# Optimization experiments

Hardware: AMD Instinct MI355X
Metric: run time of the kernel (lower is better)

The kernel has to match this reference:

```python
import jax, jax.numpy as jnp
import numpy as np

B, D, K, E = 4096, 2048, 512, 8  # tokens, model dim, kept SVD rank, experts


def setup_inputs() -> dict:
    key = jax.random.key(0)
    ks = jax.random.split(key, 7)
    x = jax.random.normal(ks[0], (B, D), dtype=jnp.float32)
    # frozen base weight (stands in for pretrained_weight)
    W = jax.random.normal(ks[1], (D, D), dtype=jnp.float32) / np.sqrt(D)
    # frozen truncated SVD factors: U_k (D,K) left vecs, V_k (K,D) as sliced in the torch code
    U_k = jnp.linalg.qr(jax.random.normal(ks[2], (D, K), dtype=jnp.float32))[0]
    V_k = jnp.linalg.qr(jax.random.normal(ks[3], (D, K), dtype=jnp.float32))[0].T
    lambda_k = jax.random.normal(ks[4], (E, K), dtype=jnp.float32) * 0.02
    v = jnp.zeros((D,), dtype=jnp.float32)
    router_W1 = jax.random.normal(ks[5], (K, 1), dtype=jnp.float32)
    router_W2 = jax.random.normal(ks[6], (1, E), dtype=jnp.float32)
    return {"x": x, "W": W, "U_k": U_k, "V_k": V_k, "lambda_k": lambda_k,
            "v": v, "router_W1": router_W1, "router_W2": router_W2}


def reference(x, W, U_k, V_k, lambda_k, v, router_W1, router_W2):
    # routing: x @ U_k -> rank-1 router -> softmax over experts
    routing = x @ U_k                                   # (B,K)
    g = jax.nn.softmax((routing @ router_W1) @ router_W2, axis=-1)  # (B,E)
    # per-expert low-rank delta weight, materialized as in the original
    delta_W = jnp.einsum('dk,ek,kn->edn', U_k, lambda_k, V_k)       # (E,D,D)
    W_tot = W[None] + delta_W                           # (E,D,D)
    # F.linear semantics: out = x @ W_tot^T per expert
    expert_out = jnp.einsum('bd,end->ben', x, W_tot)    # (B,E,D)
    out = jnp.einsum('ben,be->bn', expert_out, g)       # gated combine
    return out * (1.0 + v)
```

## Files before the change

### kernel.cpp

```cpp
#include <hip/hip_runtime.h>
#include <hip/hip_bf16.h>
#include <cstdint>

#define B_TOK 4096
#define DDIM  2048
#define KR    512
#define NE    8

using f32x4  = __attribute__((ext_vector_type(4))) float;
using short8 = __attribute__((ext_vector_type(8))) short;
using u16 = unsigned short;

__device__ inline u16 f2bf(float f) {
    union { float f; uint32_t u; } x; x.f = f;
    uint32_t u = x.u;
    return (u16)((u + 0x7fffu + ((u >> 16) & 1u)) >> 16);
}

__device__ inline void gload_lds16(const u16* g, u16* l) {
    __builtin_amdgcn_global_load_lds(
        (const __attribute__((address_space(1))) void*)g,
        (__attribute__((address_space(3))) void*)l, 16, 0, 0);
}

__global__ void cvt_copy2d(const float* __restrict__ src, u16* __restrict__ dst,
                           int rows, int cols4, int src_ld, int dst_ld) {
    int total = rows * cols4;
    for (int i = blockIdx.x * blockDim.x + threadIdx.x; i < total;
         i += gridDim.x * blockDim.x) {
        int r = i / cols4, c = i - r * cols4;
        float4 val = *((const float4*)(src + (size_t)r * src_ld) + c);
        ushort4 o;
        o.x = f2bf(val.x); o.y = f2bf(val.y); o.z = f2bf(val.z); o.w = f2bf(val.w);
        *((ushort4*)(dst + (size_t)r * dst_ld) + c) = o;
    }
}

__global__ void transpose_cvt(const float* __restrict__ src, u16* __restrict__ dst,
                              int src_cols , int dst_ld ) {
    __shared__ float tile[32][33];
    int c0 = blockIdx.x * 32;
    int r0 = blockIdx.y * 32;
    int tx = threadIdx.x, ty = threadIdx.y;
    #pragma unroll
    for (int j = 0; j < 32; j += 8)
        tile[ty + j][tx] = src[(size_t)(r0 + ty + j) * src_cols + c0 + tx];
    __syncthreads();
    #pragma unroll
    for (int j = 0; j < 32; j += 8)
        dst[(size_t)(c0 + ty + j) * dst_ld + r0 + tx] = f2bf(tile[tx][ty + j]);
}

__global__ __launch_bounds__(256)
void router_kernel(const float* __restrict__ rt, const float* __restrict__ W1,
                   const float* __restrict__ W2, const float* __restrict__ lam,
                   u16* __restrict__ Aaug) {
    int b = blockIdx.x;
    int tid = threadIdx.x;
    const float* r = rt + (size_t)b * 1024;

    float p = r[tid] * W1[tid] + r[tid + 256] * W1[tid + 256];
    #pragma unroll
    for (int o = 32; o > 0; o >>= 1) p += __shfl_down(p, o);
    __shared__ float sp[4];
    __shared__ float sbc;
    if ((tid & 63) == 0) sp[tid >> 6] = p;
    __syncthreads();
    if (tid == 0) sbc = sp[0] + sp[1] + sp[2] + sp[3];
    __syncthreads();
    float s = sbc;

    float g[NE]; float mx = -1e30f;
    #pragma unroll
    for (int e = 0; e < NE; e++) { g[e] = s * W2[e]; mx = fmaxf(mx, g[e]); }
    float den = 0.f;
    #pragma unroll
    for (int e = 0; e < NE; e++) { g[e] = expf(g[e] - mx); den += g[e]; }
    float inv = 1.0f / den;

    for (int kk = tid; kk < KR; kk += 256) {
        float mu = 0.f;
        #pragma unroll
        for (int e = 0; e < NE; e++) mu += g[e] * lam[e * KR + kk];
        float m = mu * inv * r[512 + kk];
        Aaug[(size_t)b * 2560 + 2048 + kk] = f2bf(m);
    }
}

template<int BM, int BN, int WGM, int WGN, bool HAS_V>
__global__ __launch_bounds__(256, 2)
void gemm_db(const u16* __restrict__ A, const u16* __restrict__ Bm,
             float* __restrict__ C, const float* __restrict__ v,
             int N, int Kc, int lda, int ldb, int nbx) {
    constexpr int MF = BM / (WGM * 16);
    constexpr int NF = BN / (WGN * 16);
    constexpr int ISSA = BM / 32;
    constexpr int ISSB = BN / 32;
    __shared__ u16 sA[2 * BM * 64];
    __shared__ u16 sB[2 * BN * 64];

    const int tid = threadIdx.x;
    const int wid = tid >> 6, lane = tid & 63;
    const int l15 = lane & 15, l4 = lane >> 4;
    const int wm = wid / WGN, wn = wid % WGN;

    const int nwg = gridDim.x;
    const int id = (blockIdx.x & 7) * (nwg >> 3) + (blockIdx.x >> 3);
    const int row0 = (id / nbx) * BM;
    const int col0 = (id % nbx) * BN;

    const int srow = tid >> 3;
    const int scol = ((tid & 7) ^ (srow & 7)) << 3;
    const u16* gA = A + (size_t)(row0 + srow) * lda + scol;
    const u16* gB = Bm + (size_t)(col0 + srow) * ldb + scol;

    f32x4 acc[MF][NF] = {};
    const int nt = Kc >> 6;

    #pragma unroll
    for (int i = 0; i < ISSA; i++)
        gload_lds16(gA + (size_t)i * 32 * lda, sA + i * 2048 + wid * 512);
    #pragma unroll
    for (int i = 0; i < ISSB; i++)
        gload_lds16(gB + (size_t)i * 32 * ldb, sB + i * 2048 + wid * 512);
    __syncthreads();

    for (int t = 0; t < nt; ++t) {
        const int cur = t & 1;
        if (t + 1 < nt) {
            const int nxt = cur ^ 1;
            const u16* gAk = gA + (size_t)(t + 1) * 64;
            const u16* gBk = gB + (size_t)(t + 1) * 64;
            #pragma unroll
            for (int i = 0; i < ISSA; i++)
                gload_lds16(gAk + (size_t)i * 32 * lda,
                            sA + nxt * BM * 64 + i * 2048 + wid * 512);
            #pragma unroll
            for (int i = 0; i < ISSB; i++)
                gload_lds16(gBk + (size_t)i * 32 * ldb,
                            sB + nxt * BN * 64 + i * 2048 + wid * 512);
        }
        const u16* a0 = sA + cur * BM * 64;
        const u16* b0 = sB + cur * BN * 64;
        #pragma unroll
        for (int kc = 0; kc < 8; kc += 4) {
            short8 af[MF], bv[NF];
            #pragma unroll
            for (int mf = 0; mf < MF; mf++) {
                int row = wm * MF * 16 + mf * 16 + l15;
                int ch = (kc + l4) ^ (row & 7);
                af[mf] = *(const short8*)(a0 + row * 64 + ch * 8);
            }
            #pragma unroll
            for (int nf = 0; nf < NF; nf++) {
                int row = wn * NF * 16 + nf * 16 + l15;
                int ch = (kc + l4) ^ (row & 7);
                bv[nf] = *(const short8*)(b0 + row * 64 + ch * 8);
            }
            #pragma unroll
            for (int mf = 0; mf < MF; mf++)
                #pragma unroll
                for (int nf = 0; nf < NF; nf++)
                    acc[mf][nf] = __builtin_amdgcn_mfma_f32_16x16x32_bf16(
                        af[mf], bv[nf], acc[mf][nf], 0, 0, 0);
        }
        __syncthreads();
    }

    #pragma unroll
    for (int nf = 0; nf < NF; nf++) {
        int col = col0 + wn * NF * 16 + nf * 16 + l15;
        float sc = HAS_V ? (1.0f + v[col]) : 1.0f;
        #pragma unroll
        for (int mf = 0; mf < MF; mf++) {
            int row = row0 + wm * MF * 16 + mf * 16 + l4 * 4;
            #pragma unroll
            for (int r2 = 0; r2 < 4; r2++)
                C[(size_t)(row + r2) * N + col] = acc[mf][nf][r2] * sc;
        }
    }
}

extern "C" void kernel_launch(void* const* d_in, const int* in_sizes, int n_in,
                              void* d_out, int out_size, void* d_ws, size_t ws_size,
                              hipStream_t stream) {
    const float* x   = (const float*)d_in[0];
    const float* W   = (const float*)d_in[1];
    const float* U   = (const float*)d_in[2];
    const float* V   = (const float*)d_in[3];
    const float* lam = (const float*)d_in[4];
    const float* v   = (const float*)d_in[5];
    const float* W1  = (const float*)d_in[6];
    const float* W2  = (const float*)d_in[7];
    float* out = (float*)d_out;

    char* ws = (char*)d_ws;
    u16*   Aaug = (u16*)ws;
    u16*   BigB = (u16*)(ws + 20971520);
    u16*   UVT  = (u16*)(ws + 31457280);
    float* rt   = (float*)(ws + 35651584);

    cvt_copy2d<<<2048, 256, 0, stream>>>(x, Aaug, 4096, 512, 2048, 2560);
    cvt_copy2d<<<2048, 256, 0, stream>>>(W, BigB, 2048, 512, 2048, 2560);
    cvt_copy2d<<<1024, 256, 0, stream>>>(U, BigB + 2048, 2048, 128, 512, 2560);
    cvt_copy2d<<<2048, 256, 0, stream>>>(V, UVT + (size_t)512 * 2048, 512, 512, 2048, 2048);
    transpose_cvt<<<dim3(16, 64), dim3(32, 8), 0, stream>>>(U, UVT, 512, 2048);

    gemm_db<128, 64, 4, 1, false><<<512, 256, 0, stream>>>(
        Aaug, UVT, rt, nullptr, 1024, 2048, 2560, 2048, 16);

    router_kernel<<<4096, 256, 0, stream>>>(rt, W1, W2, lam, Aaug);

    gemm_db<128, 128, 2, 2, true><<<512, 256, 0, stream>>>(
        Aaug, BigB, out, v, 2048, 2560, 2560, 2560, 16);
}
```

Measured before the change: 111.1 us.

## Fold router projection into U·W1 vector, shrink first GEMM, add triple-buffered main GEMM

Precomputes u1 = U_k @ router_W1 so the router scalar becomes a dot product of x with a vector. The first GEMM then only computes x @ V_k^T (N=512 instead of 1024), and the U-transpose kernel is dropped. The main GEMM moves to a new 256x128-tile, 512-thread kernel with a three-slot LDS ring, explicit vmcnt waits and s_setprio around the MFMA block. This cuts first-GEMM work and aims for better latency hiding in the dominant GEMM, at the cost of one block per CU and hand-written waitcnt assumptions.

Result: faster. 106.4 us (-4.3%).

```diff
diff --git a/kernel.cpp b/kernel.cpp
--- a/kernel.cpp
+++ b/kernel.cpp
@@ -15,6 +15,10 @@
     union { float f; uint32_t u; } x; x.f = f;
     uint32_t u = x.u;
     return (u16)((u + 0x7fffu + ((u >> 16) & 1u)) >> 16);
+}
+__device__ inline float bf2f(u16 h) {
+    union { uint32_t u; float f; } x; x.u = ((uint32_t)h) << 16;
+    return x.f;
 }
 
 __device__ inline void gload_lds16(const u16* g, u16* l) {
@@ -36,37 +40,40 @@
     }
 }
 
-__global__ void transpose_cvt(const float* __restrict__ src, u16* __restrict__ dst,
-                              int src_cols , int dst_ld ) {
-    __shared__ float tile[32][33];
-    int c0 = blockIdx.x * 32;
-    int r0 = blockIdx.y * 32;
-    int tx = threadIdx.x, ty = threadIdx.y;
-    #pragma unroll
-    for (int j = 0; j < 32; j += 8)
-        tile[ty + j][tx] = src[(size_t)(r0 + ty + j) * src_cols + c0 + tx];
+__global__ __launch_bounds__(64)
+void uw1_kernel(const float* __restrict__ U, const float* __restrict__ W1,
+                float* __restrict__ u1) {
+    int d = blockIdx.x, lane = threadIdx.x;
+    const float* row = U + (size_t)d * KR;
+    float s = 0.f;
+    #pragma unroll
+    for (int k = 0; k < KR; k += 64) s += row[k + lane] * W1[k + lane];
+    #pragma unroll
+    for (int o = 32; o > 0; o >>= 1) s += __shfl_down(s, o);
+    if (lane == 0) u1[d] = s;
+}
+
+__global__ __launch_bounds__(256)
+void router2(const u16* __restrict__ Ax, const float* __restrict__ u1,
+             const float* __restrict__ W2, const float* __restrict__ lam,
+             const float* __restrict__ tmat, u16* __restrict__ Am) {
+    int b = blockIdx.x, tid = threadIdx.x;
+    const u16* xr = Ax + (size_t)b * 2560;
+
+    short8 xv = *(const short8*)(xr + tid * 8);
+    float4 ua = *((const float4*)(u1 + tid * 8));
+    float4 ub = *((const float4*)(u1 + tid * 8) + 1);
+    float p = bf2f((u16)xv[0]) * ua.x + bf2f((u16)xv[1]) * ua.y +
+              bf2f((u16)xv[2]) * ua.z + bf2f((u16)xv[3]) * ua.w +
+              bf2f((u16)xv[4]) * ub.x + bf2f((u16)xv[5]) * ub.y +
+              bf2f((u16)xv[6]) * ub.z + bf2f((u16)xv[7]) * ub.w;
+    #pragma unroll
+    for (int o = 32; o > 0; o >>= 1) p += __shfl_down(p, o);
+    __shared__ float sp4[4];
+    __shared__ float sbc;
+    if ((tid & 63) == 0) sp4[tid >> 6] = p;
     __syncthreads();
-    #pragma unroll
-    for (int j = 0; j < 32; j += 8)
-        dst[(size_t)(c0 + ty + j) * dst_ld + r0 + tx] = f2bf(tile[tx][ty + j]);
-}
-
-__global__ __launch_bounds__(256)
-void router_kernel(const float* __restrict__ rt, const float* __restrict__ W1,
-                   const float* __restrict__ W2, const float* __restrict__ lam,
-                   u16* __restrict__ Aaug) {
-    int b = blockIdx.x;
-    int tid = threadIdx.x;
-    const float* r = rt + (size_t)b * 1024;
-
-    float p = r[tid] * W1[tid] + r[tid + 256] * W1[tid + 256];
-    #pragma unroll
-    for (int o = 32; o > 0; o >>= 1) p += __shfl_down(p, o);
-    __shared__ float sp[4];
-    __shared__ float sbc;
-    if ((tid & 63) == 0) sp[tid >> 6] = p;
-    __syncthreads();
-    if (tid == 0) sbc = sp[0] + sp[1] + sp[2] + sp[3];
+    if (tid == 0) sbc = sp4[0] + sp4[1] + sp4[2] + sp4[3];
     __syncthreads();
     float s = sbc;
 
@@ -82,8 +89,8 @@
         float mu = 0.f;
         #pragma unroll
         for (int e = 0; e < NE; e++) mu += g[e] * lam[e * KR + kk];
-        float m = mu * inv * r[512 + kk];
-        Aaug[(size_t)b * 2560 + 2048 + kk] = f2bf(m);
+        Am[(size_t)b * 2560 + 2048 + kk] =
+            f2bf(mu * inv * tmat[(size_t)b * KR + kk]);
     }
 }
 
@@ -177,6 +184,123 @@
             #pragma unroll
             for (int r2 = 0; r2 < 4; r2++)
                 C[(size_t)(row + r2) * N + col] = acc[mf][nf][r2] * sc;
+        }
+    }
+}
+
+template<int BM, int BN, int WGM, int WGN, bool HAS_V>
+__global__ __launch_bounds__(WGM * WGN * 64, 1)
+void gemm_ring(const u16* __restrict__ A, const u16* __restrict__ Bm,
+               float* __restrict__ C, const float* __restrict__ v,
+               int N, int Kc, int lda, int ldb, int nbx) {
+    constexpr int NT = WGM * WGN * 64;
+    constexpr int MF = BM / (WGM * 16);
+    constexpr int NF = BN / (WGN * 16);
+    constexpr int SLOT = (BM + BN) * 64;
+    constexpr int ROWS = NT / 8;
+    constexpr int ISSA = BM / ROWS;
+    constexpr int ISSB = BN / ROWS;
+    static_assert(ISSA + ISSB == 6, "vmcnt literals assume 6 loads/tile");
+    __shared__ u16 lds[3 * SLOT];
+
+    const int tid = threadIdx.x;
+    const int wid = tid >> 6, lane = tid & 63;
+    const int l15 = lane & 15, l4 = lane >> 4;
+    const int wm = wid / WGN, wn = wid % WGN;
+
+    const int nwg = gridDim.x;
+    const int id = (blockIdx.x & 7) * (nwg >> 3) + (blockIdx.x >> 3);
+    const int row0 = (id / nbx) * BM;
+    const int col0 = (id % nbx) * BN;
+
+    const int srow = tid >> 3;
+    const int scol = ((tid & 7) ^ (srow & 7)) << 3;
+    const u16* gA = A + (size_t)(row0 + srow) * lda + scol;
+    const u16* gB = Bm + (size_t)(col0 + srow) * ldb + scol;
+
+    f32x4 acc[MF][NF] = {};
+    const int nt = Kc >> 6;
+
+    #pragma unroll
+    for (int p = 0; p < 2; p++) {
+        const u16* gAt = gA + p * 64;
+        const u16* gBt = gB + p * 64;
+        u16* sl = lds + p * SLOT;
+        #pragma unroll
+        for (int i = 0; i < ISSA; i++)
+            gload_lds16(gAt + (size_t)i * ROWS * lda,
+                        sl + i * ROWS * 64 + wid * 512);
+        #pragma unroll
+        for (int i = 0; i < ISSB; i++)
+            gload_lds16(gBt + (size_t)i * ROWS * ldb,
+                        sl + BM * 64 + i * ROWS * 64 + wid * 512);
+    }
+    asm volatile("s_waitcnt vmcnt(6)" ::: "memory");
+    __builtin_amdgcn_s_barrier();
+    asm volatile("" ::: "memory");
+
+    int sc = 0, sp = 2;
+    for (int t = 0; t < nt; ++t) {
+        if (t + 2 < nt) {
+            const u16* gAt = gA + (size_t)(t + 2) * 64;
+            const u16* gBt = gB + (size_t)(t + 2) * 64;
+            u16* sl = lds + sp * SLOT;
+            #pragma unroll
+            for (int i = 0; i < ISSA; i++)
+                gload_lds16(gAt + (size_t)i * ROWS * lda,
+                            sl + i * ROWS * 64 + wid * 512);
+            #pragma unroll
+            for (int i = 0; i < ISSB; i++)
+                gload_lds16(gBt + (size_t)i * ROWS * ldb,
+                            sl + BM * 64 + i * ROWS * 64 + wid * 512);
+        }
+        const u16* a0 = lds + sc * SLOT;
+        const u16* b0 = a0 + BM * 64;
+        __builtin_amdgcn_s_setprio(1);
+        #pragma unroll
+        for (int kc = 0; kc < 8; kc += 4) {
+            short8 af[MF], bv[NF];
+            #pragma unroll
+            for (int mf = 0; mf < MF; mf++) {
+                int row = wm * MF * 16 + mf * 16 + l15;
+                int ch = (kc + l4) ^ (row & 7);
+                af[mf] = *(const short8*)(a0 + row * 64 + ch * 8);
+            }
+            #pragma unroll
+            for (int nf = 0; nf < NF; nf++) {
+                int row = wn * NF * 16 + nf * 16 + l15;
+                int ch = (kc + l4) ^ (row & 7);
+                bv[nf] = *(const short8*)(b0 + row * 64 + ch * 8);
+            }
+            #pragma unroll
+            for (int mf = 0; mf < MF; mf++)
+                #pragma unroll
+                for (int nf = 0; nf < NF; nf++)
+                    acc[mf][nf] = __builtin_amdgcn_mfma_f32_16x16x32_bf16(
+                        af[mf], bv[nf], acc[mf][nf], 0, 0, 0);
+        }
+        __builtin_amdgcn_s_setprio(0);
+
+        const int rem = nt - 1 - t;
+        if (rem == 0) break;
+        if (rem >= 2) asm volatile("s_waitcnt vmcnt(6)" ::: "memory");
+        else          asm volatile("s_waitcnt vmcnt(0)" ::: "memory");
+        __builtin_amdgcn_s_barrier();
+        asm volatile("" ::: "memory");
+        sc = (sc == 2) ? 0 : sc + 1;
+        sp = (sp == 2) ? 0 : sp + 1;
+    }
+
+    #pragma unroll
+    for (int nf = 0; nf < NF; nf++) {
+        int col = col0 + wn * NF * 16 + nf * 16 + l15;
+        float sc2 = HAS_V ? (1.0f + v[col]) : 1.0f;
+        #pragma unroll
+        for (int mf = 0; mf < MF; mf++) {
+            int row = row0 + wm * MF * 16 + mf * 16 + l4 * 4;
+            #pragma unroll
+            for (int r2 = 0; r2 < 4; r2++)
+                C[(size_t)(row + r2) * N + col] = acc[mf][nf][r2] * sc2;
         }
     }
 }
@@ -197,20 +321,21 @@
     char* ws = (char*)d_ws;
     u16*   Aaug = (u16*)ws;
     u16*   BigB = (u16*)(ws + 20971520);
-    u16*   UVT  = (u16*)(ws + 31457280);
-    float* rt   = (float*)(ws + 35651584);
+    u16*   Vb   = (u16*)(ws + 31457280);
+    float* tmat = (float*)(ws + 33554432);
+    float* u1   = (float*)(ws + 41943040);
 
     cvt_copy2d<<<2048, 256, 0, stream>>>(x, Aaug, 4096, 512, 2048, 2560);
     cvt_copy2d<<<2048, 256, 0, stream>>>(W, BigB, 2048, 512, 2048, 2560);
     cvt_copy2d<<<1024, 256, 0, stream>>>(U, BigB + 2048, 2048, 128, 512, 2560);
-    cvt_copy2d<<<2048, 256, 0, stream>>>(V, UVT + (size_t)512 * 2048, 512, 512, 2048, 2048);
-    transpose_cvt<<<dim3(16, 64), dim3(32, 8), 0, stream>>>(U, UVT, 512, 2048);
-
-    gemm_db<128, 64, 4, 1, false><<<512, 256, 0, stream>>>(
-        Aaug, UVT, rt, nullptr, 1024, 2048, 2560, 2048, 16);
-
-    router_kernel<<<4096, 256, 0, stream>>>(rt, W1, W2, lam, Aaug);
-
-    gemm_db<128, 128, 2, 2, true><<<512, 256, 0, stream>>>(
+    cvt_copy2d<<<1024, 256, 0, stream>>>(V, Vb, 512, 512, 2048, 2048);
+    uw1_kernel<<<2048, 64, 0, stream>>>(U, W1, u1);
+
+    gemm_db<128, 64, 4, 1, false><<<256, 256, 0, stream>>>(
+        Aaug, Vb, tmat, nullptr, 512, 2048, 2560, 2048, 8);
+
+    router2<<<4096, 256, 0, stream>>>(Aaug, u1, W2, lam, tmat, Aaug);
+
+    gemm_ring<256, 128, 4, 2, true><<<256, 512, 0, stream>>>(
         Aaug, BigB, out, v, 2048, 2560, 2560, 2560, 16);
 }
```
